# Performance work log

Hardware: AMD Instinct MI355X
Metric: run time of the kernel (lower is better)

The kernel has to match this reference:

```python
import jax, jax.numpy as jnp
import numpy as np

N_TOKENS = 32768
HIDDEN = 2048
NUM_EXPERTS = 64
TOP_K = 2


def setup_inputs() -> dict:
    key = jax.random.key(0)
    kx, kw = jax.random.split(key)
    x = jax.random.normal(kx, (N_TOKENS, HIDDEN), dtype=jnp.float32)
    # nn.Linear weight init scale ~ 1/sqrt(fan_in)
    gate_w = jax.random.normal(kw, (HIDDEN, NUM_EXPERTS), dtype=jnp.float32) / np.sqrt(HIDDEN)
    return {"x": x, "gate_w": gate_w}


def reference(x, gate_w):
    # logits: [N, E]
    logits = x @ gate_w
    # top-k over experts
    top_k_logits, top_k_indices = jax.lax.top_k(logits, TOP_K)  # [N, K]
    top_k_weights = jax.nn.softmax(top_k_logits, axis=-1)        # [N, K]
    probs = jax.nn.softmax(logits, axis=-1)                      # [N, E]
    # per-expert routed-token counts via segment-sum over flattened top-k indices
    tokens_per_expert = jax.ops.segment_sum(
        jnp.ones((x.shape[0] * TOP_K,), dtype=x.dtype),
        top_k_indices.reshape(-1),
        num_segments=NUM_EXPERTS,
    )
    f = tokens_per_expert / max(x.shape[0], 1)   # fraction of tokens per expert
    P = probs.mean(axis=0)                        # mean router prob per expert
    load_balance_loss = NUM_EXPERTS * jnp.sum(f * P)
    return top_k_weights, top_k_indices, load_balance_loss
```

## Files before the change

kernel.cpp:

```cpp
#include <hip/hip_runtime.h>
#include <math.h>

#define N_TOKENS 32768
#define HIDDEN   2048
#define NEXP     64
#define BM 64
#define NWAVE 4
#define NBLK (N_TOKENS / BM)
#define KSLICE (HIDDEN / NWAVE)
#define KSTEP 32
#define NSTEP (KSLICE / KSTEP)
#define WV_F 4096
#define ARENA_F 16640
#define XSCALE 64.f
#define WSCALE 256.f
#define DESCALE (1.f / 16384.f)

typedef __attribute__((ext_vector_type(8))) _Float16 half8;
typedef __attribute__((ext_vector_type(4))) float f32x4;

__device__ __forceinline__ void gload16(const void* g, void* l) {
    __builtin_amdgcn_global_load_lds(
        (const __attribute__((address_space(1))) void*)g,
        (__attribute__((address_space(3))) void*)l, 16, 0, 0);
}

__global__ void wsplit_kernel(const float* __restrict__ gw,
                              _Float16* __restrict__ wh, _Float16* __restrict__ wl) {
    const int S   = blockIdx.x;
    const int tid = threadIdx.x;
    const int nt  = tid >> 6;
    const int l   = tid & 63;
    const int col = nt * 16 + (l & 15);
    const int krow = 32 * S + (l >> 4) * 8;
    half8 vh, vl;
    #pragma unroll
    for (int j = 0; j < 8; ++j) {
        const float w = gw[(size_t)(krow + j) * NEXP + col] * WSCALE;
        const _Float16 hh = (_Float16)w;
        vh[j] = hh;
        vl[j] = (_Float16)(w - (float)hh);
    }
    const size_t off = ((size_t)(S * 4 + nt) * 64 + l) * 8;
    *reinterpret_cast<half8*>(wh + off) = vh;
    *reinterpret_cast<half8*>(wl + off) = vl;
}

__global__ __launch_bounds__(256, 2)
void router_main(const float* __restrict__ x,
                 const _Float16* __restrict__ whp, const _Float16* __restrict__ wlp,
                 float* __restrict__ out_w, float* __restrict__ out_i,
                 float* __restrict__ wsP, int* __restrict__ wsC)
{
    __shared__ __align__(16) float arena[ARENA_F];
    __shared__ float pred[NWAVE][NEXP];
    __shared__ int   cntl[NEXP];

    const int tid  = threadIdx.x;
    const int lane = tid & 63;
    const int rw   = __builtin_amdgcn_readfirstlane(tid >> 6);
    const int m0   = blockIdx.x * BM;
    if (tid < NEXP) cntl[tid] = 0;

    float* const xt = arena + rw * WV_F;
    float* const bt = xt + 2048;

    const int stok = lane >> 3;
    const int su   = (lane & 7) ^ stok;

    f32x4 acc[4][4];
    const f32x4 zero = {0.f, 0.f, 0.f, 0.f};
    #pragma unroll
    for (int mt = 0; mt < 4; ++mt)
        #pragma unroll
        for (int nt = 0; nt < 4; ++nt) acc[mt][nt] = zero;

    for (int s = 0; s < NSTEP; ++s) {
        const int k0 = rw * KSLICE + s * KSTEP;
        asm volatile("s_waitcnt lgkmcnt(0)" ::: "memory");
        #pragma unroll
        for (int i = 0; i < 8; ++i) {
            const float* g = x + (size_t)(m0 + i * 8 + stok) * HIDDEN + k0 + su * 4;
            gload16(g, xt + i * 256);
        }
        const _Float16* bh = whp + (size_t)(rw * NSTEP + s) * 2048;
        const _Float16* bl = wlp + (size_t)(rw * NSTEP + s) * 2048;
        #pragma unroll
        for (int q = 0; q < 4; ++q) gload16(bh + q * 512 + lane * 8, bt + q * 256);
        #pragma unroll
        for (int q = 0; q < 4; ++q) gload16(bl + q * 512 + lane * 8, bt + 1024 + q * 256);
        asm volatile("s_waitcnt vmcnt(0)" ::: "memory");
        __builtin_amdgcn_sched_barrier(0);

        half8 bfh[4], bfl[4];
        #pragma unroll
        for (int nt = 0; nt < 4; ++nt) {
            bfh[nt] = *reinterpret_cast<const half8*>(bt + nt * 256 + lane * 4);
            bfl[nt] = *reinterpret_cast<const half8*>(bt + 1024 + nt * 256 + lane * 4);
        }
        half8 afh[4], afl[4];
        #pragma unroll
        for (int mt = 0; mt < 4; ++mt) {
            const int tok = mt * 16 + (lane & 15);
            const int t7  = lane & 7;
            const int vb  = (lane >> 4) * 2;
            const float* xrow = xt + tok * 32;
            const f32x4 q0 = *reinterpret_cast<const f32x4*>(xrow + ((vb ^ t7) << 2));
            const f32x4 q1 = *reinterpret_cast<const f32x4*>(xrow + (((vb + 1) ^ t7) << 2));
            half8 ah, al;
            #pragma unroll
            for (int j = 0; j < 4; ++j) {
                const float v = q0[j] * XSCALE;
                const _Float16 hh = (_Float16)v;
                ah[j] = hh; al[j] = (_Float16)(v - (float)hh);
            }
            #pragma unroll
            for (int j = 0; j < 4; ++j) {
                const float v = q1[j] * XSCALE;
                const _Float16 hh = (_Float16)v;
                ah[4 + j] = hh; al[4 + j] = (_Float16)(v - (float)hh);
            }
            afh[mt] = ah; afl[mt] = al;
        }
        #pragma unroll
        for (int mt = 0; mt < 4; ++mt)
            #pragma unroll
            for (int nt = 0; nt < 4; ++nt) {
                f32x4 c = acc[mt][nt];
                c = __builtin_amdgcn_mfma_f32_16x16x32_f16(afh[mt], bfh[nt], c, 0, 0, 0);
                c = __builtin_amdgcn_mfma_f32_16x16x32_f16(afh[mt], bfl[nt], c, 0, 0, 0);
                c = __builtin_amdgcn_mfma_f32_16x16x32_f16(afl[mt], bfh[nt], c, 0, 0, 0);
                acc[mt][nt] = c;
            }
    }

    __syncthreads();

    {
        float* part = arena + rw * (BM * 65);
        #pragma unroll
        for (int mt = 0; mt < 4; ++mt)
            #pragma unroll
            for (int nt = 0; nt < 4; ++nt)
                #pragma unroll
                for (int r = 0; r < 4; ++r)
                    part[(mt * 16 + (lane >> 4) * 4 + r) * 65 + nt * 16 + (lane & 15)] =
                        acc[mt][nt][r] * DESCALE;
    }
    __syncthreads();

    float sumP = 0.f;
    for (int t = 0; t < 16; ++t) {
        const int m = rw * 16 + t;
        float l = 0.f;
        #pragma unroll
        for (int s2 = 0; s2 < NWAVE; ++s2)
            l += arena[s2 * (BM * 65) + m * 65 + lane];

        float v = l; int idx = lane;
        #pragma unroll
        for (int off = 32; off >= 1; off >>= 1) {
            float ov = __shfl_xor(v, off);
            int   oi = __shfl_xor(idx, off);
            if (ov > v || (ov == v && oi < idx)) { v = ov; idx = oi; }
        }
        const float v1 = v; const int i1 = idx;
        v = (lane == i1) ? -INFINITY : l;
        idx = lane;
        #pragma unroll
        for (int off = 32; off >= 1; off >>= 1) {
            float ov = __shfl_xor(v, off);
            int   oi = __shfl_xor(idx, off);
            if (ov > v || (ov == v && oi < idx)) { v = ov; idx = oi; }
        }
        const float v2 = v; const int i2 = idx;
        const float ed  = expf(v2 - v1);
        const float wt1 = 1.f / (1.f + ed);
        const float wt2 = ed / (1.f + ed);
        const float p = expf(l - v1);
        float Z = p;
        #pragma unroll
        for (int off = 32; off >= 1; off >>= 1) Z += __shfl_xor(Z, off);
        sumP += p / Z;
        if (lane == 0) {
            const size_t o = (size_t)(m0 + m) * 2;
            out_w[o]     = wt1;
            out_w[o + 1] = wt2;
            out_i[o]     = (float)i1;
            out_i[o + 1] = (float)i2;
            atomicAdd(&cntl[i1], 1);
            atomicAdd(&cntl[i2], 1);
        }
    }
    pred[rw][lane] = sumP;
    __syncthreads();
    if (tid < NEXP) {
        float s = 0.f;
        #pragma unroll
        for (int w2 = 0; w2 < NWAVE; ++w2) s += pred[w2][tid];
        wsP[(size_t)blockIdx.x * NEXP + tid] = s;
        wsC[(size_t)blockIdx.x * NEXP + tid] = cntl[tid];
    }
}

__global__ void router_finalize(const float* __restrict__ wsP, const int* __restrict__ wsC,
                                float* __restrict__ out_loss)
{
    const int e = threadIdx.x;
    float P = 0.f, C = 0.f;
    for (int b = 0; b < NBLK; ++b) {
        P += wsP[(size_t)b * NEXP + e];
        C += (float)wsC[(size_t)b * NEXP + e];
    }
    float val = (C / (float)N_TOKENS) * (P / (float)N_TOKENS);
    #pragma unroll
    for (int off = 32; off >= 1; off >>= 1) val += __shfl_xor(val, off);
    if (e == 0) out_loss[0] = (float)NEXP * val;
}

extern "C" void kernel_launch(void* const* d_in, const int* in_sizes, int n_in,
                              void* d_out, int out_size, void* d_ws, size_t ws_size,
                              hipStream_t stream) {
    const float* x  = (const float*)d_in[0];
    const float* gw = (const float*)d_in[1];
    float* out   = (float*)d_out;
    float* out_w = out;
    float* out_i = out + (size_t)N_TOKENS * 2;
    float* loss  = out + (size_t)N_TOKENS * 4;
    float*    wsP = (float*)d_ws;
    int*      wsC = (int*)((char*)d_ws + 131072);
    _Float16* wh  = (_Float16*)((char*)d_ws + 262144);
    _Float16* wl  = wh + (size_t)HIDDEN * NEXP;
    hipLaunchKernelGGL(wsplit_kernel, dim3(HIDDEN / KSTEP), dim3(256), 0, stream, gw, wh, wl);
    hipLaunchKernelGGL(router_main, dim3(NBLK), dim3(256), 0, stream,
                       x, wh, wl, out_w, out_i, wsP, wsC);
    hipLaunchKernelGGL(router_finalize, dim3(1), dim3(64), 0, stream, wsP, wsC, loss);
}
```

Measured before the change: 99.78 us.

## Split waves by token rows with shared double-buffered weight tiles

Each wave now owns 16 token rows across the full hidden dimension, where before each wave took a K-slice for all 64 rows. Global-to-LDS loads are double-buffered so the next K-step is prefetched while MFMAs run on the current one, and the weight tile is loaded cooperatively and shared by all waves. This removes the cross-wave partial-sum reduction and shrinks LDS use, which may raise occupancy. The cost is two workgroup barriers per K-step and a longer serial K loop per wave. The finalize loop also gets an unroll pragma.

```diff
diff --git a/kernel.cpp b/kernel.cpp
--- a/kernel.cpp
+++ b/kernel.cpp
@@ -7,14 +7,12 @@
 #define BM 64
 #define NWAVE 4
 #define NBLK (N_TOKENS / BM)
-#define KSLICE (HIDDEN / NWAVE)
 #define KSTEP 32
-#define NSTEP (KSLICE / KSTEP)
-#define WV_F 4096
-#define ARENA_F 16640
+#define NSTEP (HIDDEN / KSTEP)
 #define XSCALE 64.f
 #define WSCALE 256.f
 #define DESCALE (1.f / 16384.f)
+#define LGS 68
 
 typedef __attribute__((ext_vector_type(8))) _Float16 half8;
 typedef __attribute__((ext_vector_type(4))) float f32x4;
@@ -52,7 +50,7 @@
                  float* __restrict__ out_w, float* __restrict__ out_i,
                  float* __restrict__ wsP, int* __restrict__ wsC)
 {
-    __shared__ __align__(16) float arena[ARENA_F];
+    __shared__ __align__(16) float arena[8192];
     __shared__ float pred[NWAVE][NEXP];
     __shared__ int   cntl[NEXP];
 
@@ -62,49 +60,57 @@
     const int m0   = blockIdx.x * BM;
     if (tid < NEXP) cntl[tid] = 0;
 
-    float* const xt = arena + rw * WV_F;
-    float* const bt = xt + 2048;
+    _Float16* const bt = reinterpret_cast<_Float16*>(arena);
+    float* const at    = arena + 4096;
 
     const int stok = lane >> 3;
     const int su   = (lane & 7) ^ stok;
 
-    f32x4 acc[4][4];
+    f32x4 acc[4];
     const f32x4 zero = {0.f, 0.f, 0.f, 0.f};
     #pragma unroll
-    for (int mt = 0; mt < 4; ++mt)
-        #pragma unroll
-        for (int nt = 0; nt < 4; ++nt) acc[mt][nt] = zero;
+    for (int nt = 0; nt < 4; ++nt) acc[nt] = zero;
+
+    #define STAGE(s, b)                                                                 \
+        {                                                                               \
+            const int k0_ = (s) * KSTEP;                                                \
+            _Pragma("unroll")                                                           \
+            for (int i = 0; i < 2; ++i) {                                               \
+                const float* g_ = x + (size_t)(m0 + rw * 16 + i * 8 + stok) * HIDDEN    \
+                                    + k0_ + su * 4;                                     \
+                gload16(g_, at + ((b) * 4 + rw) * 512 + i * 256);                       \
+            }                                                                           \
+            gload16(whp + ((size_t)((s) * 4 + rw) * 64 + lane) * 8,                     \
+                    bt + (((b) * 2 + 0) * 4 + rw) * 512);                               \
+            gload16(wlp + ((size_t)((s) * 4 + rw) * 64 + lane) * 8,                     \
+                    bt + (((b) * 2 + 1) * 4 + rw) * 512);                               \
+        }
+
+    STAGE(0, 0);
 
     for (int s = 0; s < NSTEP; ++s) {
-        const int k0 = rw * KSLICE + s * KSTEP;
-        asm volatile("s_waitcnt lgkmcnt(0)" ::: "memory");
-        #pragma unroll
-        for (int i = 0; i < 8; ++i) {
-            const float* g = x + (size_t)(m0 + i * 8 + stok) * HIDDEN + k0 + su * 4;
-            gload16(g, xt + i * 256);
-        }
-        const _Float16* bh = whp + (size_t)(rw * NSTEP + s) * 2048;
-        const _Float16* bl = wlp + (size_t)(rw * NSTEP + s) * 2048;
-        #pragma unroll
-        for (int q = 0; q < 4; ++q) gload16(bh + q * 512 + lane * 8, bt + q * 256);
-        #pragma unroll
-        for (int q = 0; q < 4; ++q) gload16(bl + q * 512 + lane * 8, bt + 1024 + q * 256);
-        asm volatile("s_waitcnt vmcnt(0)" ::: "memory");
+        const int b = s & 1;
+        if (s + 1 < NSTEP) {
+            STAGE(s + 1, b ^ 1);
+            asm volatile("s_waitcnt vmcnt(4)" ::: "memory");
+        } else {
+            asm volatile("s_waitcnt vmcnt(0)" ::: "memory");
+        }
         __builtin_amdgcn_sched_barrier(0);
+        __builtin_amdgcn_s_barrier();
 
         half8 bfh[4], bfl[4];
         #pragma unroll
         for (int nt = 0; nt < 4; ++nt) {
-            bfh[nt] = *reinterpret_cast<const half8*>(bt + nt * 256 + lane * 4);
-            bfl[nt] = *reinterpret_cast<const half8*>(bt + 1024 + nt * 256 + lane * 4);
-        }
-        half8 afh[4], afl[4];
-        #pragma unroll
-        for (int mt = 0; mt < 4; ++mt) {
-            const int tok = mt * 16 + (lane & 15);
+            bfh[nt] = *reinterpret_cast<const half8*>(bt + ((b * 2 + 0) * 4 + nt) * 512 + lane * 8);
+            bfl[nt] = *reinterpret_cast<const half8*>(bt + ((b * 2 + 1) * 4 + nt) * 512 + lane * 8);
+        }
+        {
+            const float* abase = at + (b * 4 + rw) * 512;
+            const int row = lane & 15;
             const int t7  = lane & 7;
             const int vb  = (lane >> 4) * 2;
-            const float* xrow = xt + tok * 32;
+            const float* xrow = abase + row * 32;
             const f32x4 q0 = *reinterpret_cast<const f32x4*>(xrow + ((vb ^ t7) << 2));
             const f32x4 q1 = *reinterpret_cast<const f32x4*>(xrow + (((vb + 1) ^ t7) << 2));
             half8 ah, al;
@@ -120,42 +126,32 @@
                 const _Float16 hh = (_Float16)v;
                 ah[4 + j] = hh; al[4 + j] = (_Float16)(v - (float)hh);
             }
-            afh[mt] = ah; afl[mt] = al;
-        }
-        #pragma unroll
-        for (int mt = 0; mt < 4; ++mt)
             #pragma unroll
             for (int nt = 0; nt < 4; ++nt) {
-                f32x4 c = acc[mt][nt];
-                c = __builtin_amdgcn_mfma_f32_16x16x32_f16(afh[mt], bfh[nt], c, 0, 0, 0);
-                c = __builtin_amdgcn_mfma_f32_16x16x32_f16(afh[mt], bfl[nt], c, 0, 0, 0);
-                c = __builtin_amdgcn_mfma_f32_16x16x32_f16(afl[mt], bfh[nt], c, 0, 0, 0);
-                acc[mt][nt] = c;
+                f32x4 c = acc[nt];
+                c = __builtin_amdgcn_mfma_f32_16x16x32_f16(ah, bfh[nt], c, 0, 0, 0);
+                c = __builtin_amdgcn_mfma_f32_16x16x32_f16(ah, bfl[nt], c, 0, 0, 0);
+                c = __builtin_amdgcn_mfma_f32_16x16x32_f16(al, bfh[nt], c, 0, 0, 0);
+                acc[nt] = c;
             }
-    }
-
-    __syncthreads();
-
-    {
-        float* part = arena + rw * (BM * 65);
-        #pragma unroll
-        for (int mt = 0; mt < 4; ++mt)
-            #pragma unroll
-            for (int nt = 0; nt < 4; ++nt)
-                #pragma unroll
-                for (int r = 0; r < 4; ++r)
-                    part[(mt * 16 + (lane >> 4) * 4 + r) * 65 + nt * 16 + (lane & 15)] =
-                        acc[mt][nt][r] * DESCALE;
-    }
+        }
+        asm volatile("s_waitcnt lgkmcnt(0)" ::: "memory");
+        __builtin_amdgcn_sched_barrier(0);
+        __builtin_amdgcn_s_barrier();
+    }
+
+    #pragma unroll
+    for (int nt = 0; nt < 4; ++nt)
+        #pragma unroll
+        for (int r = 0; r < 4; ++r)
+            arena[(rw * 16 + (lane >> 4) * 4 + r) * LGS + nt * 16 + (lane & 15)] =
+                acc[nt][r] * DESCALE;
     __syncthreads();
 
     float sumP = 0.f;
     for (int t = 0; t < 16; ++t) {
         const int m = rw * 16 + t;
-        float l = 0.f;
-        #pragma unroll
-        for (int s2 = 0; s2 < NWAVE; ++s2)
-            l += arena[s2 * (BM * 65) + m * 65 + lane];
+        const float l = arena[m * LGS + lane];
 
         float v = l; int idx = lane;
         #pragma unroll
@@ -208,6 +204,7 @@
 {
     const int e = threadIdx.x;
     float P = 0.f, C = 0.f;
+    #pragma unroll 8
     for (int b = 0; b < NBLK; ++b) {
         P += wsP[(size_t)b * NEXP + e];
         C += (float)wsC[(size_t)b * NEXP + e];
```

Result: slower. 113.5 us (+13.8%).
